# Optimization experiments

Measured on AMD Instinct MI355X. Metric: run time of the kernel, lower is better.

## Reference

```python
import jax, jax.numpy as jnp
import numpy as np

D_MODEL, D_FF, N_EXPERTS, P = 512, 2048, 16, 128
B, S = 8, 512


def setup_inputs() -> dict:
    key = jax.random.key(0)
    ks = jax.random.split(key, 16)
    T = B * S
    g = lambda k, shape, fan: (jax.random.normal(k, shape, jnp.float32) * (fan ** -0.5))
    return {
        "x": jax.random.normal(ks[0], (B, S, D_MODEL), jnp.float32),
        "h_prev": jax.random.normal(ks[1], (T, P), jnp.float32),
        # projector: Linear(d_model -> p)
        "Wp": g(ks[2], (P, D_MODEL), D_MODEL), "bp": jnp.zeros((P,), jnp.float32),
        # GRUCell(p, p): torch layout [3p, p] in (r, z, n) order
        "W_ih": g(ks[3], (3 * P, P), P), "W_hh": g(ks[4], (3 * P, P), P),
        "b_ih": jnp.zeros((3 * P,), jnp.float32), "b_hh": jnp.zeros((3 * P,), jnp.float32),
        # router: Linear(p -> num_experts)
        "Wr": g(ks[5], (N_EXPERTS, P), P), "br": jnp.zeros((N_EXPERTS,), jnp.float32),
        # experts: Linear(d, dff) -> ReLU -> Linear(dff, d), stacked over experts
        "W1": g(ks[6], (N_EXPERTS, D_MODEL, D_FF), D_MODEL),
        "b1": jnp.zeros((N_EXPERTS, D_FF), jnp.float32),
        "W2": g(ks[7], (N_EXPERTS, D_FF, D_MODEL), D_FF),
        "b2": jnp.zeros((N_EXPERTS, D_MODEL), jnp.float32),
        "k": 2,
    }


def reference(x, h_prev, Wp, bp, W_ih, W_hh, b_ih, b_hh, Wr, br, W1, b1, W2, b2, k):
    Bsz, Seq, d = x.shape
    xf = x.reshape(-1, d)                      # [T, d]
    xp = xf @ Wp.T + bp                        # [T, p]
    # GRUCell (torch semantics, gate order r,z,n)
    gx = xp @ W_ih.T + b_ih                    # [T, 3p]
    gh = h_prev @ W_hh.T + b_hh                # [T, 3p]
    xr, xz, xn = jnp.split(gx, 3, axis=-1)
    hr, hz, hn = jnp.split(gh, 3, axis=-1)
    r = jax.nn.sigmoid(xr + hr)
    z = jax.nn.sigmoid(xz + hz)
    n = jnp.tanh(xn + r * hn)
    h = (1.0 - z) * n + z * h_prev             # [T, p]
    # router -> top-k, renormalized
    probs = jax.nn.softmax(h @ Wr.T + br, axis=-1)       # [T, E]
    top_p, top_i = jax.lax.top_k(probs, k)               # [T, k]
    top_p = top_p / jnp.sum(top_p, axis=-1, keepdims=True)
    T = xf.shape[0]
    E = Wr.shape[0]
    # dense combine weights: cw[t, e] = renorm prob if e in top-k else 0
    cw = jnp.zeros((T, E), x.dtype).at[jnp.arange(T)[:, None], top_i].set(top_p)
    out = jnp.zeros_like(xf)
    for e in range(E):  # fixed small expert count; per-expert GEMM, masked combine
        y = jax.nn.relu(xf @ W1[e] + b1[e]) @ W2[e] + b2[e]
        out = out + cw[:, e:e + 1] * y
    return out.reshape(Bsz, Seq, d), h
```

## Files before the change

### kernel.cpp

```cpp
#include <hip/hip_runtime.h>
#include <cmath>

#define T_TOK 4096
#define DM    512
#define DFF   2048
#define NE    16
#define PP    128

typedef __attribute__((ext_vector_type(8))) short bfrag;
typedef __attribute__((ext_vector_type(4))) float f32x4;
typedef __attribute__((ext_vector_type(8))) unsigned short us8;

__device__ __forceinline__ unsigned short f2bf(float f) {
  unsigned int u = __float_as_uint(f);
  unsigned int r = (u + 0x7FFFu + ((u >> 16) & 1u)) >> 16;
  return (unsigned short)r;
}
__device__ __forceinline__ float bf2f(unsigned short b) {
  return __uint_as_float(((unsigned int)b) << 16);
}

#define GLOAD_LDS16(g, l) __builtin_amdgcn_global_load_lds( \
    (const __attribute__((address_space(1))) void*)(g), \
    (__attribute__((address_space(3))) void*)(l), 16, 0, 0)

__global__ __launch_bounds__(256) void sgemm_nt_bias(
    const float* __restrict__ A, const float* __restrict__ B,
    const float* __restrict__ bias, float* __restrict__ C,
    int M, int N, int K)
{
  __shared__ __align__(16) float As[16][68];
  __shared__ __align__(16) float Bs[16][68];
  const int bm = blockIdx.x * 64;
  const int bn = blockIdx.y * 64;
  const int tid = threadIdx.x;
  const int tx = tid & 15;
  const int ty = tid >> 4;

  float acc[4][4] = {{0.f}};

  for (int k0 = 0; k0 < K; k0 += 16) {
    {
      int r  = tid >> 2;
      int c4 = (tid & 3) * 4;
      float4 v = *(const float4*)(A + (size_t)(bm + r) * K + k0 + c4);
      As[c4+0][r] = v.x; As[c4+1][r] = v.y; As[c4+2][r] = v.z; As[c4+3][r] = v.w;
    }
    {
      int r  = tid >> 2;
      int c4 = (tid & 3) * 4;
      float4 v = *(const float4*)(B + (size_t)(bn + r) * K + k0 + c4);
      Bs[c4+0][r] = v.x; Bs[c4+1][r] = v.y; Bs[c4+2][r] = v.z; Bs[c4+3][r] = v.w;
    }
    __syncthreads();
    #pragma unroll
    for (int k = 0; k < 16; ++k) {
      float4 a4 = *(const float4*)&As[k][ty*4];
      float4 b4 = *(const float4*)&Bs[k][tx*4];
      float a[4] = {a4.x, a4.y, a4.z, a4.w};
      float b[4] = {b4.x, b4.y, b4.z, b4.w};
      #pragma unroll
      for (int i = 0; i < 4; ++i)
        #pragma unroll
        for (int j = 0; j < 4; ++j)
          acc[i][j] += a[i] * b[j];
    }
    __syncthreads();
  }
  #pragma unroll
  for (int i = 0; i < 4; ++i) {
    int row = bm + ty*4 + i;
    #pragma unroll
    for (int j = 0; j < 4; ++j) {
      int col = bn + tx*4 + j;
      C[(size_t)row * N + col] = acc[i][j] + bias[col];
    }
  }
}

__global__ __launch_bounds__(256) void sgemm_cat(
    const float* __restrict__ A1, const float* __restrict__ A2,
    const float* __restrict__ B, const float* __restrict__ bias,
    float* __restrict__ C)
{
  __shared__ __align__(16) float As[16][68];
  __shared__ __align__(16) float Bs[16][68];
  const int bm = blockIdx.x * 64;
  const int bn = blockIdx.y * 64;
  const int tid = threadIdx.x;
  const int tx = tid & 15;
  const int ty = tid >> 4;

  float acc[4][4] = {{0.f}};

  for (int k0 = 0; k0 < 256; k0 += 16) {
    {
      int r  = tid >> 2;
      int c4 = (tid & 3) * 4;
      const float* src = (k0 < 128) ? (A1 + (size_t)(bm + r) * 128 + k0 + c4)
                                    : (A2 + (size_t)(bm + r) * 128 + (k0 - 128) + c4);
      float4 v = *(const float4*)src;
      As[c4+0][r] = v.x; As[c4+1][r] = v.y; As[c4+2][r] = v.z; As[c4+3][r] = v.w;
    }
    {
      int r  = tid >> 2;
      int c4 = (tid & 3) * 4;
      float4 v = *(const float4*)(B + (size_t)(bn + r) * 256 + k0 + c4);
      Bs[c4+0][r] = v.x; Bs[c4+1][r] = v.y; Bs[c4+2][r] = v.z; Bs[c4+3][r] = v.w;
    }
    __syncthreads();
    #pragma unroll
    for (int k = 0; k < 16; ++k) {
      float4 a4 = *(const float4*)&As[k][ty*4];
      float4 b4 = *(const float4*)&Bs[k][tx*4];
      float a[4] = {a4.x, a4.y, a4.z, a4.w};
      float b[4] = {b4.x, b4.y, b4.z, b4.w};
      #pragma unroll
      for (int i = 0; i < 4; ++i)
        #pragma unroll
        for (int j = 0; j < 4; ++j)
          acc[i][j] += a[i] * b[j];
    }
    __syncthreads();
  }
  #pragma unroll
  for (int i = 0; i < 4; ++i) {
    int row = bm + ty*4 + i;
    #pragma unroll
    for (int j = 0; j < 4; ++j) {
      int col = bn + tx*4 + j;
      C[(size_t)row * 512 + col] = acc[i][j] + bias[col];
    }
  }
}

__global__ void prep_gates(const float* __restrict__ W_ih, const float* __restrict__ W_hh,
                           const float* __restrict__ b_ih, const float* __restrict__ b_hh,
                           float* __restrict__ Bcat, float* __restrict__ bcat,
                           int* __restrict__ cnt)
{
  int id = blockIdx.x * 256 + threadIdx.x;
  if (blockIdx.x == 0 && threadIdx.x < NE) cnt[threadIdx.x] = 0;
  int n = id >> 8, k = id & 255;
  float v;
  if (n < 256)      v = (k < 128) ? W_ih[n * 128 + k] : W_hh[n * 128 + k - 128];
  else if (n < 384) v = (k < 128) ? W_ih[n * 128 + k] : 0.f;
  else              v = (k < 128) ? 0.f : W_hh[(n - 128) * 128 + k - 128];
  Bcat[n * 256 + k] = v;
  if (id < 512) {
    float b = (id < 256) ? (b_ih[id] + b_hh[id])
            : (id < 384) ? b_ih[id] : b_hh[id - 128];
    bcat[id] = b;
  }
}

__global__ void gru_elem2(const float* __restrict__ s, const float* __restrict__ hprev,
                          float* __restrict__ hout)
{
  int i = blockIdx.x * blockDim.x + threadIdx.x;
  int t = i >> 7, p = i & 127;
  const float* sr = s + (size_t)t * 512;
  float rz = sr[p], zz = sr[128 + p], xn = sr[256 + p], hn = sr[384 + p];
  float r = 1.f / (1.f + expf(-rz));
  float z = 1.f / (1.f + expf(-zz));
  float n = tanhf(xn + r * hn);
  hout[i] = (1.f - z) * n + z * hprev[i];
}

__global__ __launch_bounds__(64) void router_topk2(
    const float* __restrict__ h, const float* __restrict__ Wr,
    const float* __restrict__ br,
    float* __restrict__ wgt, int* __restrict__ tokslot,
    int* __restrict__ cnt)
{
  __shared__ float4 wr4[NE * 32];
  __shared__ float br_s[NE];
  __shared__ int hist[NE];
  __shared__ int basex[NE];

  int tid = threadIdx.x;
  #pragma unroll
  for (int i = 0; i < 8; ++i)
    wr4[tid + i * 64] = ((const float4*)Wr)[tid + i * 64];
  if (tid < NE) { br_s[tid] = br[tid]; hist[tid] = 0; }
  __syncthreads();

  int t = blockIdx.x * 64 + tid;
  const float4* hr = (const float4*)(h + (size_t)t * PP);

  float logit[NE];
  #pragma unroll
  for (int e = 0; e < NE; ++e) logit[e] = 0.f;
  #pragma unroll 4
  for (int i = 0; i < 32; ++i) {
    float4 v = hr[i];
    #pragma unroll
    for (int e = 0; e < NE; ++e) {
      float4 w = wr4[e * 32 + i];
      logit[e] += v.x * w.x + v.y * w.y + v.z * w.z + v.w * w.w;
    }
  }
  #pragma unroll
  for (int e = 0; e < NE; ++e) logit[e] += br_s[e];

  float mx = logit[0];
  #pragma unroll
  for (int e = 1; e < NE; ++e) mx = fmaxf(mx, logit[e]);
  float p[NE];
  #pragma unroll
  for (int e = 0; e < NE; ++e) p[e] = expf(logit[e] - mx);
  int i0 = 0; float m0 = p[0];
  #pragma unroll
  for (int e = 1; e < NE; ++e) { if (p[e] > m0) { m0 = p[e]; i0 = e; } }
  int i1 = -1; float m1 = -1.f;
  #pragma unroll
  for (int e = 0; e < NE; ++e) { if (e != i0 && p[e] > m1) { m1 = p[e]; i1 = e; } }
  float inv = 1.f / (m0 + m1);
  float w0 = m0 * inv, w1 = m1 * inv;

  int r0 = atomicAdd(&hist[i0], 1);
  int r1 = atomicAdd(&hist[i1], 1);
  __syncthreads();
  if (tid < NE && hist[tid] > 0) basex[tid] = atomicAdd(&cnt[tid], hist[tid]);
  __syncthreads();

  int p0 = basex[i0] + r0;
  tokslot[(size_t)i0 * T_TOK + p0] = (t << 1);
  wgt[(size_t)i0 * T_TOK + p0] = w0;
  int p1 = basex[i1] + r1;
  tokslot[(size_t)i1 * T_TOK + p1] = (t << 1) | 1;
  wgt[(size_t)i1 * T_TOK + p1] = w1;
}

__global__ void calc_off(const int* __restrict__ cnt, int* __restrict__ offPad) {
  if (threadIdx.x == 0) {
    int s = 0;
    for (int e = 0; e < NE; ++e) { offPad[e] = s; s += (cnt[e] + 127) & ~127; }
    offPad[NE] = s;
  }
}

__global__ __launch_bounds__(256) void transpose_cvt(
    const float* __restrict__ in, unsigned short* __restrict__ out, int K, int N)
{
  __shared__ float tl[64][65];
  int e = blockIdx.z, kt = blockIdx.y, nt = blockIdx.x;
  const float* ib = in + (size_t)e * K * N + (size_t)(kt * 64) * N + nt * 64;
  int t = threadIdx.x;
  int r = t >> 2, c0 = (t & 3) * 16;
  #pragma unroll
  for (int i = 0; i < 4; ++i) {
    float4 v = *(const float4*)(ib + (size_t)r * N + c0 + i * 4);
    tl[r][c0+i*4+0] = v.x; tl[r][c0+i*4+1] = v.y;
    tl[r][c0+i*4+2] = v.z; tl[r][c0+i*4+3] = v.w;
  }
  __syncthreads();
  unsigned short* ob = out + (size_t)e * N * K + (size_t)(nt * 64) * K + kt * 64;
  #pragma unroll
  for (int i = 0; i < 2; ++i) {
    int u = t + i * 256;
    int n = u >> 3, k0 = (u & 7) * 8;
    us8 o;
    #pragma unroll
    for (int j = 0; j < 8; ++j) o[j] = f2bf(tl[k0 + j][n]);
    *(us8*)(ob + (size_t)n * K + k0) = o;
  }
}

__global__ __launch_bounds__(256) void gather_x(
    const float* __restrict__ x, const int* __restrict__ tokslot,
    const int* __restrict__ cnt, const int* __restrict__ offPad,
    unsigned short* __restrict__ xg)
{
  int e = blockIdx.y;
  int n = cnt[e];
  int npad = (n + 127) & ~127;
  int r0 = blockIdx.x * 128;
  if (r0 >= npad) return;
  int t = threadIdx.x;
  int r = r0 + (t >> 1);
  int half = t & 1;
  unsigned short* orow = xg + (size_t)(offPad[e] + r) * DM + half * 256;
  if (r >= n) {
    us8 z = {0,0,0,0,0,0,0,0};
    #pragma unroll
    for (int i = 0; i < 32; ++i) *(us8*)(orow + i * 8) = z;
    return;
  }
  int tok = tokslot[(size_t)e * T_TOK + r] >> 1;
  const float* irow = x + (size_t)tok * DM + half * 256;
  #pragma unroll
  for (int i = 0; i < 32; ++i) {
    float4 a = *(const float4*)(irow + i * 8);
    float4 b = *(const float4*)(irow + i * 8 + 4);
    us8 o;
    o[0]=f2bf(a.x); o[1]=f2bf(a.y); o[2]=f2bf(a.z); o[3]=f2bf(a.w);
    o[4]=f2bf(b.x); o[5]=f2bf(b.y); o[6]=f2bf(b.z); o[7]=f2bf(b.w);
    *(us8*)(orow + i * 8) = o;
  }
}

__global__ __launch_bounds__(512, 4) void expert_gemm1(
    const unsigned short* __restrict__ xg, const unsigned short* __restrict__ W1t,
    const float* __restrict__ b1,
    const int* __restrict__ cnt, const int* __restrict__ offPad,
    unsigned short* __restrict__ hidden)
{
  __shared__ unsigned short wlds[64 * 512];
  int bid = blockIdx.x;
  int xcd = bid & 7, j = bid >> 3;
  int e  = xcd * 2 + (j >> 5);
  int nb = (j & 31) * 64;
  int t = threadIdx.x, lane = t & 63, wv = t >> 6;
  int l15 = lane & 15, lg = lane >> 4;
  int wm = wv * 32;

  const unsigned short* w1b = W1t + ((size_t)e * DFF + nb) * DM;
  #pragma unroll
  for (int i = 0; i < 8; ++i) {
    int s = t + i * 512;
    int r = s >> 6, c = s & 63;
    int cs = (c & 56) | ((c & 7) ^ (r & 7));
    GLOAD_LDS16(w1b + (size_t)r * DM + (cs << 3), &wlds[s * 8]);
  }
  __syncthreads();

  int npad = (cnt[e] + 127) & ~127;
  int ebase = offPad[e];

  for (int tb = 0; tb < npad; tb += 256) {
    int roff[2];
    #pragma unroll
    for (int fi = 0; fi < 2; ++fi) {
      int r0 = wm + fi * 16;
      roff[fi] = (tb + r0 >= npad) ? r0 - 128 : r0;
    }
    f32x4 acc[2][4];
    #pragma unroll
    for (int i = 0; i < 2; ++i)
      #pragma unroll
      for (int jj = 0; jj < 4; ++jj) acc[i][jj] = (f32x4){0.f, 0.f, 0.f, 0.f};

    #pragma unroll 2
    for (int kt = 0; kt < 8; ++kt) {
      #pragma unroll
      for (int kk = 0; kk < 2; ++kk) {
        int cidx = kt * 8 + kk * 4 + lg;
        bfrag a[2], b[4];
        #pragma unroll
        for (int fi = 0; fi < 2; ++fi)
          a[fi] = *(const bfrag*)(xg + (size_t)(ebase + tb + roff[fi] + l15) * DM + (cidx << 3));
        #pragma unroll
        for (int fj = 0; fj < 4; ++fj) {
          int row = fj * 16 + l15;
          int cs = (cidx & 56) | ((cidx & 7) ^ (row & 7));
          b[fj] = *(const bfrag*)&wlds[row * 512 + (cs << 3)];
        }
        #pragma unroll
        for (int fi = 0; fi < 2; ++fi)
          #pragma unroll
          for (int fj = 0; fj < 4; ++fj)
            acc[fi][fj] = __builtin_amdgcn_mfma_f32_16x16x32_bf16(a[fi], b[fj], acc[fi][fj], 0, 0, 0);
      }
    }

    #pragma unroll
    for (int fj = 0; fj < 4; ++fj) {
      int col = nb + fj * 16 + l15;
      float bias = b1[(size_t)e * DFF + col];
      #pragma unroll
      for (int fi = 0; fi < 2; ++fi) {
        #pragma unroll
        for (int rg = 0; rg < 4; ++rg) {
          int row = ebase + tb + roff[fi] + lg * 4 + rg;
          float v = acc[fi][fj][rg] + bias;
          hidden[(size_t)row * DFF + col] = f2bf(v > 0.f ? v : 0.f);
        }
      }
    }
  }
}

__global__ __launch_bounds__(512, 4) void expert_gemm2(
    const unsigned short* __restrict__ hidden, const unsigned short* __restrict__ W2t,
    const float* __restrict__ b2,
    const int* __restrict__ cnt, const int* __restrict__ offPad,
    const int* __restrict__ tokslot, const float* __restrict__ wgt,
    unsigned short* __restrict__ planes)
{
  __shared__ unsigned short wlds[64 * 512];
  int bid = blockIdx.x;
  int xcd = bid & 7, j = bid >> 3;
  int e   = xcd * 2 + (j >> 5);
  int r5  = j & 31;
  int ncb = (r5 & 7) * 64;
  int kq  = r5 >> 3;
  int kb  = kq * 512;
  int t = threadIdx.x, lane = t & 63, wv = t >> 6;
  int l15 = lane & 15, lg = lane >> 4;
  int wm = wv * 32;

  const unsigned short* w2b = W2t + ((size_t)e * DM + ncb) * DFF + kb;
  #pragma unroll
  for (int i = 0; i < 8; ++i) {
    int s = t + i * 512;
    int r = s >> 6, c = s & 63;
    int cs = (c & 56) | ((c & 7) ^ (r & 7));
    GLOAD_LDS16(w2b + (size_t)r * DFF + (cs << 3), &wlds[s * 8]);
  }
  __syncthreads();

  int n = cnt[e];
  int npad = (n + 127) & ~127;
  int ebase = offPad[e];

  for (int tb = 0; tb < npad; tb += 256) {
    int roff[2];
    #pragma unroll
    for (int fi = 0; fi < 2; ++fi) {
      int r0 = wm + fi * 16;
      roff[fi] = (tb + r0 >= npad) ? r0 - 128 : r0;
    }
    f32x4 acc[2][4];
    #pragma unroll
    for (int i = 0; i < 2; ++i)
      #pragma unroll
      for (int jj = 0; jj < 4; ++jj) acc[i][jj] = (f32x4){0.f, 0.f, 0.f, 0.f};

    #pragma unroll 2
    for (int kt = 0; kt < 8; ++kt) {
      #pragma unroll
      for (int kk = 0; kk < 2; ++kk) {
        int cidx = kt * 8 + kk * 4 + lg;
        bfrag a[2], b[4];
        #pragma unroll
        for (int fi = 0; fi < 2; ++fi)
          a[fi] = *(const bfrag*)(hidden + (size_t)(ebase + tb + roff[fi] + l15) * DFF + kb + (cidx << 3));
        #pragma unroll
        for (int fj = 0; fj < 4; ++fj) {
          int row = fj * 16 + l15;
          int cs = (cidx & 56) | ((cidx & 7) ^ (row & 7));
          b[fj] = *(const bfrag*)&wlds[row * 512 + (cs << 3)];
        }
        #pragma unroll
        for (int fi = 0; fi < 2; ++fi)
          #pragma unroll
          for (int fj = 0; fj < 4; ++fj)
            acc[fi][fj] = __builtin_amdgcn_mfma_f32_16x16x32_bf16(a[fi], b[fj], acc[fi][fj], 0, 0, 0);
      }
    }

    #pragma unroll
    for (int fi = 0; fi < 2; ++fi) {
      #pragma unroll
      for (int rg = 0; rg < 4; ++rg) {
        int idx = tb + roff[fi] + lg * 4 + rg;
        if (idx >= n) continue;
        int ts = tokslot[(size_t)e * T_TOK + idx];
        float w = wgt[(size_t)e * T_TOK + idx];
        unsigned short* pl = planes + ((size_t)(kq * 2 + (ts & 1)) * T_TOK + (ts >> 1)) * DM;
        #pragma unroll
        for (int fj = 0; fj < 4; ++fj) {
          int col = ncb + fj * 16 + l15;
          float bv = (kq == 0) ? b2[(size_t)e * DM + col] : 0.f;
          pl[col] = f2bf((acc[fi][fj][rg] + bv) * w);
        }
      }
    }
  }
}

__global__ __launch_bounds__(256) void combine_out(
    const unsigned short* __restrict__ planes, float* __restrict__ out)
{
  int i = blockIdx.x * blockDim.x + threadIdx.x;
  float s[8] = {0.f};
  #pragma unroll
  for (int pl = 0; pl < 8; ++pl) {
    us8 v = *(const us8*)&planes[(size_t)pl * T_TOK * DM + (size_t)i * 8];
    #pragma unroll
    for (int jj = 0; jj < 8; ++jj) s[jj] += bf2f(v[jj]);
  }
  float4* o = (float4*)(out + (size_t)i * 8);
  o[0] = make_float4(s[0], s[1], s[2], s[3]);
  o[1] = make_float4(s[4], s[5], s[6], s[7]);
}

extern "C" void kernel_launch(void* const* d_in, const int* in_sizes, int n_in,
                              void* d_out, int out_size, void* d_ws, size_t ws_size,
                              hipStream_t stream)
{
  const float* x      = (const float*)d_in[0];
  const float* h_prev = (const float*)d_in[1];
  const float* Wp     = (const float*)d_in[2];
  const float* bp     = (const float*)d_in[3];
  const float* W_ih   = (const float*)d_in[4];
  const float* W_hh   = (const float*)d_in[5];
  const float* b_ih   = (const float*)d_in[6];
  const float* b_hh   = (const float*)d_in[7];
  const float* Wr     = (const float*)d_in[8];
  const float* br     = (const float*)d_in[9];
  const float* W1     = (const float*)d_in[10];
  const float* b1     = (const float*)d_in[11];
  const float* W2     = (const float*)d_in[12];
  const float* b2     = (const float*)d_in[13];
  (void)in_sizes; (void)n_in; (void)out_size; (void)ws_size;

  float* out  = (float*)d_out;
  float* hout = out + (size_t)T_TOK * DM;

  char* ws = (char*)d_ws;
  unsigned short* W1t    = (unsigned short*)(ws + 0);
  unsigned short* planes = (unsigned short*)(ws + 0);
  unsigned short* W2t = (unsigned short*)(ws + 33554432);
  unsigned short* hidden = (unsigned short*)(ws + 67108864);
  float* xp   = (float*)(ws + 67108864);
  float* gs   = (float*)(ws + 69206016);
  float* Bcat = (float*)(ws + 77594624);
  float* bcat = (float*)(ws + 78118912);
  unsigned short* xg = (unsigned short*)(ws + 109051904);
  float* wgt   = (float*)(ws + 119537664);
  int* tokslot = (int*)(ws + 119799808);
  int* cnt     = (int*)(ws + 120061952);
  int* offPad  = (int*)(ws + 120062016);

  prep_gates<<<512, 256, 0, stream>>>(W_ih, W_hh, b_ih, b_hh, Bcat, bcat, cnt);
  sgemm_nt_bias<<<dim3(T_TOK/64, PP/64), 256, 0, stream>>>(x, Wp, bp, xp, T_TOK, PP, DM);
  sgemm_cat<<<dim3(T_TOK/64, 512/64), 256, 0, stream>>>(xp, h_prev, Bcat, bcat, gs);
  gru_elem2<<<(T_TOK * PP) / 256, 256, 0, stream>>>(gs, h_prev, hout);
  router_topk2<<<64, 64, 0, stream>>>(hout, Wr, br, wgt, tokslot, cnt);
  calc_off<<<1, 64, 0, stream>>>(cnt, offPad);

  transpose_cvt<<<dim3(DFF/64, DM/64, NE), 256, 0, stream>>>(W1, W1t, DM, DFF);
  transpose_cvt<<<dim3(DM/64, DFF/64, NE), 256, 0, stream>>>(W2, W2t, DFF, DM);

  gather_x<<<dim3(32, NE), 256, 0, stream>>>(x, tokslot, cnt, offPad, xg);
  expert_gemm1<<<512, 512, 0, stream>>>(xg, W1t, b1, cnt, offPad, hidden);
  expert_gemm2<<<512, 512, 0, stream>>>(hidden, W2t, b2, cnt, offPad, tokslot, wgt, planes);
  combine_out<<<(T_TOK * DM / 8) / 256, 256, 0, stream>>>(planes, out);
}
```

Measured before the change: 272.9 us.

## Fuse weight transpose and bf16 conversion into expert GEMM LDS staging

```diff
diff --git a/kernel.cpp b/kernel.cpp
--- a/kernel.cpp
+++ b/kernel.cpp
@@ -6,6 +6,7 @@
 #define DFF   2048
 #define NE    16
 #define PP    128
+#define WROW  520
 
 typedef __attribute__((ext_vector_type(8))) short bfrag;
 typedef __attribute__((ext_vector_type(4))) float f32x4;
@@ -19,10 +20,6 @@
 __device__ __forceinline__ float bf2f(unsigned short b) {
   return __uint_as_float(((unsigned int)b) << 16);
 }
-
-#define GLOAD_LDS16(g, l) __builtin_amdgcn_global_load_lds( \
-    (const __attribute__((address_space(1))) void*)(g), \
-    (__attribute__((address_space(3))) void*)(l), 16, 0, 0)
 
 __global__ __launch_bounds__(256) void sgemm_nt_bias(
     const float* __restrict__ A, const float* __restrict__ B,
@@ -240,33 +237,6 @@
   }
 }
 
-__global__ __launch_bounds__(256) void transpose_cvt(
-    const float* __restrict__ in, unsigned short* __restrict__ out, int K, int N)
-{
-  __shared__ float tl[64][65];
-  int e = blockIdx.z, kt = blockIdx.y, nt = blockIdx.x;
-  const float* ib = in + (size_t)e * K * N + (size_t)(kt * 64) * N + nt * 64;
-  int t = threadIdx.x;
-  int r = t >> 2, c0 = (t & 3) * 16;
-  #pragma unroll
-  for (int i = 0; i < 4; ++i) {
-    float4 v = *(const float4*)(ib + (size_t)r * N + c0 + i * 4);
-    tl[r][c0+i*4+0] = v.x; tl[r][c0+i*4+1] = v.y;
-    tl[r][c0+i*4+2] = v.z; tl[r][c0+i*4+3] = v.w;
-  }
-  __syncthreads();
-  unsigned short* ob = out + (size_t)e * N * K + (size_t)(nt * 64) * K + kt * 64;
-  #pragma unroll
-  for (int i = 0; i < 2; ++i) {
-    int u = t + i * 256;
-    int n = u >> 3, k0 = (u & 7) * 8;
-    us8 o;
-    #pragma unroll
-    for (int j = 0; j < 8; ++j) o[j] = f2bf(tl[k0 + j][n]);
-    *(us8*)(ob + (size_t)n * K + k0) = o;
-  }
-}
-
 __global__ __launch_bounds__(256) void gather_x(
     const float* __restrict__ x, const int* __restrict__ tokslot,
     const int* __restrict__ cnt, const int* __restrict__ offPad,
@@ -300,13 +270,13 @@
   }
 }
 
-__global__ __launch_bounds__(512, 4) void expert_gemm1(
-    const unsigned short* __restrict__ xg, const unsigned short* __restrict__ W1t,
+__global__ __launch_bounds__(512, 2) void expert_gemm1(
+    const unsigned short* __restrict__ xg, const float* __restrict__ W1,
     const float* __restrict__ b1,
     const int* __restrict__ cnt, const int* __restrict__ offPad,
     unsigned short* __restrict__ hidden)
 {
-  __shared__ unsigned short wlds[64 * 512];
+  __shared__ unsigned short wlds[64 * WROW];
   int bid = blockIdx.x;
   int xcd = bid & 7, j = bid >> 3;
   int e  = xcd * 2 + (j >> 5);
@@ -315,13 +285,18 @@
   int l15 = lane & 15, lg = lane >> 4;
   int wm = wv * 32;
 
-  const unsigned short* w1b = W1t + ((size_t)e * DFF + nb) * DM;
-  #pragma unroll
-  for (int i = 0; i < 8; ++i) {
-    int s = t + i * 512;
-    int r = s >> 6, c = s & 63;
-    int cs = (c & 56) | ((c & 7) ^ (r & 7));
-    GLOAD_LDS16(w1b + (size_t)r * DM + (cs << 3), &wlds[s * 8]);
+  {
+    const float* w1src = W1 + (size_t)e * DM * DFF + nb;
+    int c4 = (t & 15) * 4, rr = t >> 4;
+    #pragma unroll
+    for (int pass = 0; pass < 16; ++pass) {
+      int r = rr + pass * 32;
+      float4 v = *(const float4*)(w1src + (size_t)r * DFF + c4);
+      wlds[(c4+0) * WROW + r] = f2bf(v.x);
+      wlds[(c4+1) * WROW + r] = f2bf(v.y);
+      wlds[(c4+2) * WROW + r] = f2bf(v.z);
+      wlds[(c4+3) * WROW + r] = f2bf(v.w);
+    }
   }
   __syncthreads();
 
@@ -329,12 +304,12 @@
   int ebase = offPad[e];
 
   for (int tb = 0; tb < npad; tb += 256) {
-    int roff[2];
-    #pragma unroll
-    for (int fi = 0; fi < 2; ++fi) {
-      int r0 = wm + fi * 16;
-      roff[fi] = (tb + r0 >= npad) ? r0 - 128 : r0;
-    }
+    int r0 = wm, r1 = wm + 16;
+    if (tb + r0 >= npad) r0 -= 128;
+    if (tb + r1 >= npad) r1 -= 128;
+    const unsigned short* a0p = xg + (size_t)(ebase + tb + r0 + l15) * DM;
+    const unsigned short* a1p = xg + (size_t)(ebase + tb + r1 + l15) * DM;
+
     f32x4 acc[2][4];
     #pragma unroll
     for (int i = 0; i < 2; ++i)
@@ -346,49 +321,49 @@
       #pragma unroll
       for (int kk = 0; kk < 2; ++kk) {
         int cidx = kt * 8 + kk * 4 + lg;
-        bfrag a[2], b[4];
-        #pragma unroll
-        for (int fi = 0; fi < 2; ++fi)
-          a[fi] = *(const bfrag*)(xg + (size_t)(ebase + tb + roff[fi] + l15) * DM + (cidx << 3));
-        #pragma unroll
-        for (int fj = 0; fj < 4; ++fj) {
-          int row = fj * 16 + l15;
-          int cs = (cidx & 56) | ((cidx & 7) ^ (row & 7));
-          b[fj] = *(const bfrag*)&wlds[row * 512 + (cs << 3)];
-        }
-        #pragma unroll
-        for (int fi = 0; fi < 2; ++fi)
-          #pragma unroll
-          for (int fj = 0; fj < 4; ++fj)
-            acc[fi][fj] = __builtin_amdgcn_mfma_f32_16x16x32_bf16(a[fi], b[fj], acc[fi][fj], 0, 0, 0);
+        bfrag a0 = *(const bfrag*)(a0p + (cidx << 3));
+        bfrag a1 = *(const bfrag*)(a1p + (cidx << 3));
+        bfrag b0 = *(const bfrag*)&wlds[(0 * 16 + l15) * WROW + cidx * 8];
+        bfrag b1f = *(const bfrag*)&wlds[(1 * 16 + l15) * WROW + cidx * 8];
+        bfrag b2 = *(const bfrag*)&wlds[(2 * 16 + l15) * WROW + cidx * 8];
+        bfrag b3 = *(const bfrag*)&wlds[(3 * 16 + l15) * WROW + cidx * 8];
+        acc[0][0] = __builtin_amdgcn_mfma_f32_16x16x32_bf16(a0, b0,  acc[0][0], 0, 0, 0);
+        acc[0][1] = __builtin_amdgcn_mfma_f32_16x16x32_bf16(a0, b1f, acc[0][1], 0, 0, 0);
+        acc[0][2] = __builtin_amdgcn_mfma_f32_16x16x32_bf16(a0, b2,  acc[0][2], 0, 0, 0);
+        acc[0][3] = __builtin_amdgcn_mfma_f32_16x16x32_bf16(a0, b3,  acc[0][3], 0, 0, 0);
+        acc[1][0] = __builtin_amdgcn_mfma_f32_16x16x32_bf16(a1, b0,  acc[1][0], 0, 0, 0);
+        acc[1][1] = __builtin_amdgcn_mfma_f32_16x16x32_bf16(a1, b1f, acc[1][1], 0, 0, 0);
+        acc[1][2] = __builtin_amdgcn_mfma_f32_16x16x32_bf16(a1, b2,  acc[1][2], 0, 0, 0);
+        acc[1][3] = __builtin_amdgcn_mfma_f32_16x16x32_bf16(a1, b3,  acc[1][3], 0, 0, 0);
       }
     }
 
+    int roff0 = r0, roff1 = r1;
     #pragma unroll
     for (int fj = 0; fj < 4; ++fj) {
       int col = nb + fj * 16 + l15;
       float bias = b1[(size_t)e * DFF + col];
       #pragma unroll
-      for (int fi = 0; fi < 2; ++fi) {
-        #pragma unroll
-        for (int rg = 0; rg < 4; ++rg) {
-          int row = ebase + tb + roff[fi] + lg * 4 + rg;
-          float v = acc[fi][fj][rg] + bias;
-          hidden[(size_t)row * DFF + col] = f2bf(v > 0.f ? v : 0.f);
-        }
+      for (int rg = 0; rg < 4; ++rg) {
+        int rowA = ebase + tb + roff0 + lg * 4 + rg;
+        float vA = acc[0][fj][rg] + bias;
+        hidden[(size_t)rowA * DFF + col] = f2bf(vA > 0.f ? vA : 0.f);
+        int rowB = ebase + tb + roff1 + lg * 4 + rg;
+        float vB = acc[1][fj][rg] + bias;
+        hidden[(size_t)rowB * DFF + col] = f2bf(vB > 0.f ? vB : 0.f);
       }
     }
   }
 }
 
 __global__ __launch_bounds__(512, 4) void expert_gemm2(
-    const unsigned short* __restrict__ hidden, const unsigned short* __restrict__ W2t,
+    const unsigned short* __restrict__ hidden, const float* __restrict__ W2,
     const float* __restrict__ b2,
     const int* __restrict__ cnt, const int* __restrict__ offPad,
     const int* __restrict__ tokslot, const float* __restrict__ wgt,
     unsigned short* __restrict__ planes)
 {
-  __shared__ unsigned short wlds[64 * 512];
+  __shared__ unsigned short wlds[64 * WROW];
   int bid = blockIdx.x;
   int xcd = bid & 7, j = bid >> 3;
   int e   = xcd * 2 + (j >> 5);
@@ -400,13 +375,18 @@
   int l15 = lane & 15, lg = lane >> 4;
   int wm = wv * 32;
 
-  const unsigned short* w2b = W2t + ((size_t)e * DM + ncb) * DFF + kb;
-  #pragma unroll
-  for (int i = 0; i < 8; ++i) {
-    int s = t + i * 512;
-    int r = s >> 6, c = s & 63;
-    int cs = (c & 56) | ((c & 7) ^ (r & 7));
-    GLOAD_LDS16(w2b + (size_t)r * DFF + (cs << 3), &wlds[s * 8]);
+  {
+    const float* w2src = W2 + (size_t)e * DFF * DM + (size_t)kb * DM + ncb;
+    int c4 = (t & 15) * 4, fr = t >> 4;
+    #pragma unroll
+    for (int pass = 0; pass < 16; ++pass) {
+      int f = fr + pass * 32;
+      float4 v = *(const float4*)(w2src + (size_t)f * DM + c4);
+      wlds[(c4+0) * WROW + f] = f2bf(v.x);
+      wlds[(c4+1) * WROW + f] = f2bf(v.y);
+      wlds[(c4+2) * WROW + f] = f2bf(v.z);
+      wlds[(c4+3) * WROW + f] = f2bf(v.w);
+    }
   }
   __syncthreads();
 
@@ -439,8 +419,7 @@
         #pragma unroll
         for (int fj = 0; fj < 4; ++fj) {
           int row = fj * 16 + l15;
-          int cs = (cidx & 56) | ((cidx & 7) ^ (row & 7));
-          b[fj] = *(const bfrag*)&wlds[row * 512 + (cs << 3)];
+          b[fj] = *(const bfrag*)&wlds[row * WROW + cidx * 8];
         }
         #pragma unroll
         for (int fi = 0; fi < 2; ++fi)
@@ -510,19 +489,17 @@
   float* hout = out + (size_t)T_TOK * DM;
 
   char* ws = (char*)d_ws;
-  unsigned short* W1t    = (unsigned short*)(ws + 0);
   unsigned short* planes = (unsigned short*)(ws + 0);
-  unsigned short* W2t = (unsigned short*)(ws + 33554432);
-  unsigned short* hidden = (unsigned short*)(ws + 67108864);
-  float* xp   = (float*)(ws + 67108864);
-  float* gs   = (float*)(ws + 69206016);
-  float* Bcat = (float*)(ws + 77594624);
-  float* bcat = (float*)(ws + 78118912);
-  unsigned short* xg = (unsigned short*)(ws + 109051904);
-  float* wgt   = (float*)(ws + 119537664);
-  int* tokslot = (int*)(ws + 119799808);
-  int* cnt     = (int*)(ws + 120061952);
-  int* offPad  = (int*)(ws + 120062016);
+  unsigned short* hidden = (unsigned short*)(ws + 35651584);
+  unsigned short* xg     = (unsigned short*)(ws + 79691776);
+  float* xp   = (float*)(ws + 92274688);
+  float* gs   = (float*)(ws + 94371840);
+  float* Bcat = (float*)(ws + 102760448);
+  float* bcat = (float*)(ws + 103284736);
+  float* wgt  = (float*)(ws + 103809024);
+  int* tokslot = (int*)(ws + 104071168);
+  int* cnt     = (int*)(ws + 104333312);
+  int* offPad  = (int*)(ws + 104333376);
 
   prep_gates<<<512, 256, 0, stream>>>(W_ih, W_hh, b_ih, b_hh, Bcat, bcat, cnt);
   sgemm_nt_bias<<<dim3(T_TOK/64, PP/64), 256, 0, stream>>>(x, Wp, bp, xp, T_TOK, PP, DM);
@@ -531,11 +508,8 @@
   router_topk2<<<64, 64, 0, stream>>>(hout, Wr, br, wgt, tokslot, cnt);
   calc_off<<<1, 64, 0, stream>>>(cnt, offPad);
 
-  transpose_cvt<<<dim3(DFF/64, DM/64, NE), 256, 0, stream>>>(W1, W1t, DM, DFF);
-  transpose_cvt<<<dim3(DM/64, DFF/64, NE), 256, 0, stream>>>(W2, W2t, DFF, DM);
-
   gather_x<<<dim3(32, NE), 256, 0, stream>>>(x, tokslot, cnt, offPad, xg);
-  expert_gemm1<<<512, 512, 0, stream>>>(xg, W1t, b1, cnt, offPad, hidden);
-  expert_gemm2<<<512, 512, 0, stream>>>(hidden, W2t, b2, cnt, offPad, tokslot, wgt, planes);
+  expert_gemm1<<<512, 512, 0, stream>>>(xg, W1, b1, cnt, offPad, hidden);
+  expert_gemm2<<<512, 512, 0, stream>>>(hidden, W2, b2, cnt, offPad, tokslot, wgt, planes);
   combine_out<<<(T_TOK * DM / 8) / 256, 256, 0, stream>>>(planes, out);
 }
```

After: 242.7 us. -11.1%, faster.
